# Performance work log

Measured on AMD Instinct MI355X. Metric: run time of the kernel, lower is better.

The kernel has to match this reference:

```python
import jax, jax.numpy as jnp
import numpy as np

DIM = 768
HEADS = 12
HEAD_DIM = DIM // HEADS
EPS = 1e-5

def setup_inputs() -> dict:
    key = jax.random.key(0)
    ks = jax.random.split(key, 12)
    s = 1.0 / np.sqrt(DIM)
    x = jax.random.normal(ks[0], (4, 2048, DIM), dtype=jnp.float32)
    Wq = jax.random.uniform(ks[1], (DIM, DIM), jnp.float32, -s, s)
    bq = jnp.zeros((DIM,), jnp.float32)
    Wk = jax.random.uniform(ks[2], (DIM, DIM), jnp.float32, -s, s)
    bk = jnp.zeros((DIM,), jnp.float32)
    Wv = jax.random.uniform(ks[3], (DIM, DIM), jnp.float32, -s, s)
    bv = jnp.zeros((DIM,), jnp.float32)
    W1 = jax.random.uniform(ks[4], (DIM, 2 * DIM), jnp.float32, -s, s)
    b1 = jnp.zeros((2 * DIM,), jnp.float32)
    s2 = 1.0 / np.sqrt(2 * DIM)
    W2 = jax.random.uniform(ks[5], (2 * DIM, DIM), jnp.float32, -s2, s2)
    b2 = jnp.zeros((DIM,), jnp.float32)
    gamma = jnp.ones((DIM,), jnp.float32)
    beta = jnp.zeros((DIM,), jnp.float32)
    return {"x": x, "Wq": Wq, "bq": bq, "Wk": Wk, "bk": bk, "Wv": Wv, "bv": bv,
            "W1": W1, "b1": b1, "W2": W2, "b2": b2, "gamma": gamma, "beta": beta}

def reference(x, Wq, bq, Wk, bk, Wv, bv, W1, b1, W2, b2, gamma, beta):
    B, S, _ = x.shape
    # QKV projections -> (B, H, S, Dh)
    q = (x @ Wq + bq).reshape(B, S, HEADS, HEAD_DIM).transpose(0, 2, 1, 3)
    k = (x @ Wk + bk).reshape(B, S, HEADS, HEAD_DIM).transpose(0, 2, 1, 3)
    v = (x @ Wv + bv).reshape(B, S, HEADS, HEAD_DIM).transpose(0, 2, 1, 3)
    scores = jnp.einsum('bhqd,bhkd->bhqk', q, k) / jnp.sqrt(jnp.float32(HEAD_DIM))
    attn = jax.nn.softmax(scores, axis=-1)  # dropout is identity in eval
    ctx = jnp.einsum('bhqk,bhkd->bhqd', attn, v)
    ctx = ctx.transpose(0, 2, 1, 3).reshape(B, S, DIM)
    # MLP
    out = jax.nn.relu(ctx @ W1 + b1) @ W2 + b2
    # residual + LayerNorm
    h = x + out
    mu = jnp.mean(h, axis=-1, keepdims=True)
    var = jnp.mean(jnp.square(h - mu), axis=-1, keepdims=True)
    return (h - mu) * jax.lax.rsqrt(var + EPS) * gamma + beta
```

## Files before the change

### kernel.cpp

```cpp
#include <hip/hip_runtime.h>
#include <stdint.h>

#define DIM 768
#define HDIM 64
#define NHEADS 12
#define SEQ 2048
#define BATCH 4
#define NTOK (BATCH*SEQ)
#define FF 1536
#define QSCALE 0.1803368801111204f

typedef __bf16 bf16x8 __attribute__((ext_vector_type(8)));
typedef float f32x4 __attribute__((ext_vector_type(4)));
typedef unsigned short u16;
typedef unsigned int u32;

static __device__ __forceinline__ u16 f2bf(float f) {
  u32 u = __float_as_uint(f);
  u32 r = (u + 0x7fffu + ((u >> 16) & 1u)) >> 16;
  return (u16)r;
}

static __device__ __forceinline__ void async16(const void* g, void* l) {
  __builtin_amdgcn_global_load_lds(
      (const __attribute__((address_space(1))) u32*)g,
      (__attribute__((address_space(3))) u32*)l, 16, 0, 0);
}


__global__ void conv_bf16(const float* __restrict__ in, u16* __restrict__ out, int n) {
  int i = (blockIdx.x * 256 + threadIdx.x) * 4;
  if (i < n) {
    float4 f = *(const float4*)(in + i);
    uint2 o;
    o.x = (u32)f2bf(f.x) | ((u32)f2bf(f.y) << 16);
    o.y = (u32)f2bf(f.z) | ((u32)f2bf(f.w) << 16);
    *(uint2*)(out + i) = o;
  }
}

__global__ void prep_weights(const float* __restrict__ Wq, const float* __restrict__ Wk,
                             const float* __restrict__ Wv, const float* __restrict__ W1,
                             const float* __restrict__ W2, const float* __restrict__ bq,
                             const float* __restrict__ bk, const float* __restrict__ bv,
                             u16* __restrict__ Wqkvt, u16* __restrict__ W1t,
                             u16* __restrict__ W2t, float* __restrict__ bqkv) {
  const int bid = blockIdx.x;
  if (bid >= 4032) {
    int i = (bid - 4032) * 256 + threadIdx.x;
    if (i < DIM) bqkv[i] = bq[i];
    else if (i < 2 * DIM) bqkv[i] = bk[i - DIM];
    else if (i < 3 * DIM) bqkv[i] = bv[i - 2 * DIM];
    return;
  }
  const float* W; u16* dst; int K, N, tile;
  if (bid < 1728) {
    int z = bid / 576, t2 = bid - z * 576;
    W = z == 0 ? Wq : (z == 1 ? Wk : Wv);
    dst = Wqkvt + (size_t)z * DIM * DIM; K = DIM; N = DIM; tile = t2;
  } else if (bid < 2880) {
    W = W1; dst = W1t; K = DIM; N = FF; tile = bid - 1728;
  } else {
    W = W2; dst = W2t; K = FF; N = DIM; tile = bid - 2880;
  }
  const int ntx = N / 32;
  const int k0 = (tile / ntx) * 32, n0 = (tile - (tile / ntx) * ntx) * 32;
  __shared__ float t32[32][33];
  const int tx = threadIdx.x & 31, ty = threadIdx.x >> 5;
#pragma unroll
  for (int i = 0; i < 4; i++)
    t32[ty + 8 * i][tx] = W[(size_t)(k0 + ty + 8 * i) * N + n0 + tx];
  __syncthreads();
#pragma unroll
  for (int i = 0; i < 4; i++)
    dst[(size_t)(n0 + ty + 8 * i) * K + k0 + tx] = f2bf(t32[tx][ty + 8 * i]);
}


template<int MODE, int NT>
__launch_bounds__(256, 3)
__global__ void gemm128(const u16* __restrict__ A, const u16* __restrict__ Bt,
                        const float* __restrict__ bias, void* __restrict__ outp,
                        int K) {
  __shared__ u16 sA[128 * 64];
  __shared__ u16 sB[128 * 64];
  const int t = threadIdx.x;
  const int w = t >> 6;
  const int lane = t & 63;
  const int quad = lane >> 4;
  const int l15 = lane & 15;

  const int fid = blockIdx.x;
  const int xcd = fid & 7;
  const int j = fid >> 3;
  const int m0 = (xcd + 8 * (j / NT)) * 128;
  const int n0 = (j % NT) * 128;

  const int wr = (w & 1) * 64;
  const int wc = (w >> 1) * 64;

  f32x4 acc[4][4];
#pragma unroll
  for (int i = 0; i < 4; i++)
#pragma unroll
    for (int jj = 0; jj < 4; jj++) acc[i][jj] = (f32x4){0.f, 0.f, 0.f, 0.f};

  const int rowA = lane >> 3;
  const int colSw = ((lane & 7) ^ rowA) * 8;

  for (int k0 = 0; k0 < K; k0 += 64) {
    __syncthreads();
#pragma unroll
    for (int jj = 0; jj < 4; jj++) {
      int r0 = (jj * 4 + w) * 8;
      async16(A + (size_t)(m0 + r0 + rowA) * K + k0 + colSw, sA + r0 * 64);
      async16(Bt + (size_t)(n0 + r0 + rowA) * K + k0 + colSw, sB + r0 * 64);
    }
    __builtin_amdgcn_s_waitcnt(0);
    __syncthreads();
#pragma unroll
    for (int ks = 0; ks < 64; ks += 32) {
      bf16x8 a[4], b[4];
#pragma unroll
      for (int i = 0; i < 4; i++)
        a[i] = *(const bf16x8*)(sA + (wr + i * 16 + l15) * 64 +
                                ((((ks >> 3) + quad) ^ (l15 & 7)) * 8));
#pragma unroll
      for (int jj = 0; jj < 4; jj++)
        b[jj] = *(const bf16x8*)(sB + (wc + jj * 16 + l15) * 64 +
                                 ((((ks >> 3) + quad) ^ (l15 & 7)) * 8));
#pragma unroll
      for (int i = 0; i < 4; i++)
#pragma unroll
        for (int jj = 0; jj < 4; jj++)
          acc[i][jj] = __builtin_amdgcn_mfma_f32_16x16x32_bf16(a[i], b[jj], acc[i][jj], 0, 0, 0);
    }
  }

#pragma unroll
  for (int i = 0; i < 4; i++) {
#pragma unroll
    for (int jj = 0; jj < 4; jj++) {
#pragma unroll
      for (int r = 0; r < 4; r++) {
        int m = m0 + wr + i * 16 + quad * 4 + r;
        int n = n0 + wc + jj * 16 + l15;
        float v = acc[i][jj][r] + bias[n];
        if (MODE == 5) {
          int b = m >> 11, s = m & 2047;
          u16* o = (u16*)outp;
          if (n < DIM) {
            int h = n >> 6, d = n & 63;
            o[(((size_t)(b * NHEADS + h) * SEQ + s) << 6) + d] = f2bf(v * QSCALE);
          } else if (n < 2 * DIM) {
            int nn = n - DIM, h = nn >> 6, d = nn & 63;
            o[(size_t)NTOK * DIM + (((size_t)(b * NHEADS + h) * SEQ + s) << 6) + d] = f2bf(v);
          } else {
            int nn = n - 2 * DIM, h = nn >> 6, d = nn & 63;
            o[2 * (size_t)NTOK * DIM + ((size_t)(b * NHEADS + h) * HDIM + d) * SEQ + s] = f2bf(v);
          }
        } else if (MODE == 3) {
          ((u16*)outp)[(size_t)m * FF + n] = f2bf(fmaxf(v, 0.f));
        } else {
          ((float*)outp)[(size_t)m * DIM + n] = v;
        }
      }
    }
  }
}


__launch_bounds__(256, 3)
__global__ void attn(const u16* __restrict__ Q, const u16* __restrict__ Kb,
                     const u16* __restrict__ Vt, u16* __restrict__ Ctx) {
  __shared__ u16 sK[128 * 64];
  __shared__ u16 sV[64 * 128];
  __shared__ u16 sP[4][32 * 64];
  const int t = threadIdx.x, w = t >> 6, lane = t & 63;
  const int quad = lane >> 4, l15 = lane & 15;

  const int fid = blockIdx.x;
  const int xcd = fid & 7;
  const int idx = fid >> 3;
  const int bh = xcd + 8 * (idx >> 4);
  const int qb = idx & 15;
  const size_t qkbase = (size_t)bh * SEQ * HDIM;
  const int q0 = qb * 128 + w * 32;

  bf16x8 qf[2][2];
#pragma unroll
  for (int i = 0; i < 2; i++)
#pragma unroll
    for (int ks = 0; ks < 2; ks++)
      qf[i][ks] = *(const bf16x8*)(Q + qkbase + (size_t)(q0 + i * 16 + l15) * HDIM +
                                   ks * 32 + quad * 8);

  f32x4 o[2][4];
#pragma unroll
  for (int i = 0; i < 2; i++)
#pragma unroll
    for (int di = 0; di < 4; di++) o[i][di] = (f32x4){0.f, 0.f, 0.f, 0.f};
  float rs[2] = {0.f, 0.f};

  const int rowK = lane >> 3;
  const int colKsw = ((lane & 7) ^ rowK) * 8;
  const int rowVl = lane >> 4;
  const int chV = lane & 15;
  const int swz = l15 & 7;

  for (int kt = 0; kt < SEQ / 128; kt++) {
    __syncthreads();
#pragma unroll
    for (int j = 0; j < 4; j++) {
      int rk = (j * 4 + w) * 8;
      async16(Kb + qkbase + (size_t)(kt * 128 + rk + rowK) * HDIM + colKsw, sK + rk * 64);
      int rv = (j * 4 + w) * 4;
      int rV = rv + rowVl;
      int cV = (chV ^ (rV & 15)) * 8;
      async16(Vt + qkbase + (size_t)rV * SEQ + kt * 128 + cV, sV + rv * 128);
    }
    __builtin_amdgcn_s_waitcnt(0);
    __syncthreads();

    u16* pw = sP[w];
#pragma unroll
    for (int hh = 0; hh < 2; hh++) {
      f32x4 sc[2][4];
#pragma unroll
      for (int n4 = 0; n4 < 4; n4++) {
        int kr = (hh * 4 + n4) * 16;
        bf16x8 a0 = *(const bf16x8*)(sK + (kr + l15) * 64 + ((quad ^ swz) * 8));
        bf16x8 a1 = *(const bf16x8*)(sK + (kr + l15) * 64 + (((4 + quad) ^ swz) * 8));
#pragma unroll
        for (int i = 0; i < 2; i++) {
          f32x4 c = (f32x4){0.f, 0.f, 0.f, 0.f};
          c = __builtin_amdgcn_mfma_f32_16x16x32_bf16(a0, qf[i][0], c, 0, 0, 0);
          c = __builtin_amdgcn_mfma_f32_16x16x32_bf16(a1, qf[i][1], c, 0, 0, 0);
          sc[i][n4] = c;
        }
      }
#pragma unroll
      for (int i = 0; i < 2; i++) {
        int row = i * 16 + l15;
#pragma unroll
        for (int n4 = 0; n4 < 4; n4++) {
          float p0 = __builtin_amdgcn_exp2f(sc[i][n4][0]);
          float p1 = __builtin_amdgcn_exp2f(sc[i][n4][1]);
          float p2 = __builtin_amdgcn_exp2f(sc[i][n4][2]);
          float p3 = __builtin_amdgcn_exp2f(sc[i][n4][3]);
          rs[i] += (p0 + p1) + (p2 + p3);
          u32 lo = __builtin_amdgcn_perm(__float_as_uint(p1) + 0x8000u,
                                         __float_as_uint(p0) + 0x8000u, 0x07060302u);
          u32 hi = __builtin_amdgcn_perm(__float_as_uint(p3) + 0x8000u,
                                         __float_as_uint(p2) + 0x8000u, 0x07060302u);
          int cp = (n4 * 2 + (quad >> 1)) ^ swz;
          *(uint2*)(pw + row * 64 + cp * 8 + (quad & 1) * 4) = (uint2){lo, hi};
        }
      }
#pragma unroll
      for (int ks = 0; ks < 2; ks++) {
        bf16x8 ap[2];
#pragma unroll
        for (int i = 0; i < 2; i++) {
          int row = i * 16 + l15;
          int cp = (ks * 4 + quad) ^ swz;
          ap[i] = *(const bf16x8*)(pw + row * 64 + cp * 8);
        }
#pragma unroll
        for (int di = 0; di < 4; di++) {
          bf16x8 b = *(const bf16x8*)(sV + (di * 16 + l15) * 128 +
                                      (((hh * 8 + ks * 4 + quad) ^ l15) * 8));
          o[0][di] = __builtin_amdgcn_mfma_f32_16x16x32_bf16(ap[0], b, o[0][di], 0, 0, 0);
          o[1][di] = __builtin_amdgcn_mfma_f32_16x16x32_bf16(ap[1], b, o[1][di], 0, 0, 0);
        }
      }
    }
  }

  float rsum[2];
#pragma unroll
  for (int i = 0; i < 2; i++) {
    float s = rs[i];
    s += __shfl_xor(s, 16);
    s += __shfl_xor(s, 32);
    rsum[i] = s;
  }
  int b = bh / NHEADS, h = bh - b * NHEADS;
#pragma unroll
  for (int i = 0; i < 2; i++) {
#pragma unroll
    for (int r = 0; r < 4; r++) {
      float inv = 1.f / __shfl(rsum[i], quad * 4 + r);
      int q = q0 + i * 16 + quad * 4 + r;
      size_t base = (size_t)(b * SEQ + q) * DIM + h * HDIM;
#pragma unroll
      for (int di = 0; di < 4; di++)
        Ctx[base + di * 16 + l15] = f2bf(o[i][di][r] * inv);
    }
  }
}


__launch_bounds__(256)
__global__ void ln_kernel(const float* __restrict__ x, const float* __restrict__ y,
                          const float* __restrict__ gamma, const float* __restrict__ beta,
                          float* __restrict__ out) {
  const int tok = blockIdx.x * 4 + (threadIdx.x >> 6);
  const int lane = threadIdx.x & 63;
  const float4* X = (const float4*)(x + (size_t)tok * DIM);
  const float4* Y = (const float4*)(y + (size_t)tok * DIM);
  const float4* G = (const float4*)gamma;
  const float4* Bt = (const float4*)beta;
  float4* O = (float4*)(out + (size_t)tok * DIM);

  float4 h[3];
  float s = 0.f;
#pragma unroll
  for (int i = 0; i < 3; i++) {
    float4 a = X[i * 64 + lane], b = Y[i * 64 + lane];
    h[i].x = a.x + b.x; h[i].y = a.y + b.y; h[i].z = a.z + b.z; h[i].w = a.w + b.w;
    s += h[i].x + h[i].y + h[i].z + h[i].w;
  }
#pragma unroll
  for (int off = 32; off >= 1; off >>= 1) s += __shfl_xor(s, off);
  float mu = s * (1.f / DIM);
  float v = 0.f;
#pragma unroll
  for (int i = 0; i < 3; i++) {
    h[i].x -= mu; h[i].y -= mu; h[i].z -= mu; h[i].w -= mu;
    v += h[i].x * h[i].x + h[i].y * h[i].y + h[i].z * h[i].z + h[i].w * h[i].w;
  }
#pragma unroll
  for (int off = 32; off >= 1; off >>= 1) v += __shfl_xor(v, off);
  float rstd = rsqrtf(v * (1.f / DIM) + 1e-5f);
#pragma unroll
  for (int i = 0; i < 3; i++) {
    float4 g = G[i * 64 + lane], bt = Bt[i * 64 + lane];
    float4 r;
    r.x = h[i].x * rstd * g.x + bt.x;
    r.y = h[i].y * rstd * g.y + bt.y;
    r.z = h[i].z * rstd * g.z + bt.z;
    r.w = h[i].w * rstd * g.w + bt.w;
    O[i * 64 + lane] = r;
  }
}


extern "C" void kernel_launch(void* const* d_in, const int* in_sizes, int n_in,
                              void* d_out, int out_size, void* d_ws, size_t ws_size,
                              hipStream_t stream) {
  const float* x  = (const float*)d_in[0];
  const float* Wq = (const float*)d_in[1];
  const float* bq = (const float*)d_in[2];
  const float* Wk = (const float*)d_in[3];
  const float* bk = (const float*)d_in[4];
  const float* Wv = (const float*)d_in[5];
  const float* bv = (const float*)d_in[6];
  const float* W1 = (const float*)d_in[7];
  const float* b1 = (const float*)d_in[8];
  const float* W2 = (const float*)d_in[9];
  const float* b2 = (const float*)d_in[10];
  const float* gamma = (const float*)d_in[11];
  const float* beta  = (const float*)d_in[12];

  char* ws = (char*)d_ws;
  u16* xb   = (u16*)ws;           ws += (size_t)NTOK * DIM * 2;
  u16* Wqkvt = (u16*)ws;          ws += (size_t)DIM * DIM * 3 * 2;
  u16* W1t  = (u16*)ws;           ws += (size_t)DIM * FF * 2;
  u16* W2t  = (u16*)ws;           ws += (size_t)DIM * FF * 2;
  float* bqkv = (float*)ws;       ws += (size_t)3 * DIM * 4;
  u16* Qb   = (u16*)ws;           ws += (size_t)NTOK * DIM * 2;
  u16* Kbf  = (u16*)ws;           ws += (size_t)NTOK * DIM * 2;
  u16* Vtb  = (u16*)ws;           ws += (size_t)NTOK * DIM * 2;
  u16* Ctx  = (u16*)ws;           ws += (size_t)NTOK * DIM * 2;
  u16* H1   = (u16*)ws;           ws += (size_t)NTOK * FF * 2;
  float* Y2 = (float*)ws;         ws += (size_t)NTOK * DIM * 4;

  conv_bf16<<<(NTOK * DIM) / 1024, 256, 0, stream>>>(x, xb, NTOK * DIM);
  prep_weights<<<4041, 256, 0, stream>>>(Wq, Wk, Wv, W1, W2, bq, bk, bv,
                                         Wqkvt, W1t, W2t, bqkv);

  gemm128<5, 18><<<1152, 256, 0, stream>>>(xb, Wqkvt, bqkv, Qb, DIM);

  attn<<<768, 256, 0, stream>>>(Qb, Kbf, Vtb, Ctx);

  gemm128<3, 12><<<768, 256, 0, stream>>>(Ctx, W1t, b1, H1, DIM);
  gemm128<4, 6><<<384, 256, 0, stream>>>(H1, W2t, b2, Y2, FF);

  ln_kernel<<<NTOK / 4, 256, 0, stream>>>(x, Y2, gamma, beta, (float*)d_out);
}
```

Before: 309.7 us.

## Double-buffer K/V tiles in attention with async prefetch and MFMA priority

Restructures the attention main loop to use 64-key tiles in double-buffered shared memory, prefetching the next K/V tile with async global-to-LDS loads while the current one is computed. This replaces the load-wait-compute pattern that fully exposed memory latency each iteration. It also raises wave priority around the MFMA phases and swaps the manual bf16 rounding for the packed v_cvt_pk_bf16_f32 instruction. The cost is twice as many loop iterations and barriers, and correctness relies on the hand-written vmcnt wait counts.

```diff
diff --git a/kernel.cpp b/kernel.cpp
--- a/kernel.cpp
+++ b/kernel.cpp
@@ -173,8 +173,8 @@
 __launch_bounds__(256, 3)
 __global__ void attn(const u16* __restrict__ Q, const u16* __restrict__ Kb,
                      const u16* __restrict__ Vt, u16* __restrict__ Ctx) {
-  __shared__ u16 sK[128 * 64];
-  __shared__ u16 sV[64 * 128];
+  __shared__ u16 sK[2][64 * 64];
+  __shared__ u16 sV[2][64 * 64];
   __shared__ u16 sP[4][32 * 64];
   const int t = threadIdx.x, w = t >> 6, lane = t & 63;
   const int quad = lane >> 4, l15 = lane & 15;
@@ -204,78 +204,92 @@
 
   const int rowK = lane >> 3;
   const int colKsw = ((lane & 7) ^ rowK) * 8;
-  const int rowVl = lane >> 4;
-  const int chV = lane & 15;
   const int swz = l15 & 7;
 
-  for (int kt = 0; kt < SEQ / 128; kt++) {
-    __syncthreads();
-#pragma unroll
-    for (int j = 0; j < 4; j++) {
-      int rk = (j * 4 + w) * 8;
-      async16(Kb + qkbase + (size_t)(kt * 128 + rk + rowK) * HDIM + colKsw, sK + rk * 64);
-      int rv = (j * 4 + w) * 4;
-      int rV = rv + rowVl;
-      int cV = (chV ^ (rV & 15)) * 8;
-      async16(Vt + qkbase + (size_t)rV * SEQ + kt * 128 + cV, sV + rv * 128);
-    }
-    __builtin_amdgcn_s_waitcnt(0);
-    __syncthreads();
-
+#define STAGE(kt, b) do {                                                          \
+    int rr0 = w * 8, rr1 = (4 + w) * 8;                                            \
+    async16(Kb + qkbase + (size_t)((kt) * 64 + rr0 + rowK) * HDIM + colKsw,        \
+            sK[b] + rr0 * 64);                                                     \
+    async16(Vt + qkbase + (size_t)(rr0 + rowK) * SEQ + (kt) * 64 + colKsw,         \
+            sV[b] + rr0 * 64);                                                     \
+    async16(Kb + qkbase + (size_t)((kt) * 64 + rr1 + rowK) * HDIM + colKsw,        \
+            sK[b] + rr1 * 64);                                                     \
+    async16(Vt + qkbase + (size_t)(rr1 + rowK) * SEQ + (kt) * 64 + colKsw,         \
+            sV[b] + rr1 * 64);                                                     \
+  } while (0)
+
+  auto compute = [&](int cur) {
+    const u16* kb = sK[cur];
+    const u16* vb = sV[cur];
     u16* pw = sP[w];
-#pragma unroll
-    for (int hh = 0; hh < 2; hh++) {
-      f32x4 sc[2][4];
+
+    f32x4 sc[2][4];
+    __builtin_amdgcn_s_setprio(1);
+#pragma unroll
+    for (int n4 = 0; n4 < 4; n4++) {
+      int kr = n4 * 16;
+      bf16x8 a0 = *(const bf16x8*)(kb + (kr + l15) * 64 + ((quad ^ swz) * 8));
+      bf16x8 a1 = *(const bf16x8*)(kb + (kr + l15) * 64 + (((4 + quad) ^ swz) * 8));
+#pragma unroll
+      for (int i = 0; i < 2; i++) {
+        f32x4 c = (f32x4){0.f, 0.f, 0.f, 0.f};
+        c = __builtin_amdgcn_mfma_f32_16x16x32_bf16(a0, qf[i][0], c, 0, 0, 0);
+        c = __builtin_amdgcn_mfma_f32_16x16x32_bf16(a1, qf[i][1], c, 0, 0, 0);
+        sc[i][n4] = c;
+      }
+    }
+    __builtin_amdgcn_s_setprio(0);
+
+#pragma unroll
+    for (int i = 0; i < 2; i++) {
+      int row = i * 16 + l15;
 #pragma unroll
       for (int n4 = 0; n4 < 4; n4++) {
-        int kr = (hh * 4 + n4) * 16;
-        bf16x8 a0 = *(const bf16x8*)(sK + (kr + l15) * 64 + ((quad ^ swz) * 8));
-        bf16x8 a1 = *(const bf16x8*)(sK + (kr + l15) * 64 + (((4 + quad) ^ swz) * 8));
-#pragma unroll
-        for (int i = 0; i < 2; i++) {
-          f32x4 c = (f32x4){0.f, 0.f, 0.f, 0.f};
-          c = __builtin_amdgcn_mfma_f32_16x16x32_bf16(a0, qf[i][0], c, 0, 0, 0);
-          c = __builtin_amdgcn_mfma_f32_16x16x32_bf16(a1, qf[i][1], c, 0, 0, 0);
-          sc[i][n4] = c;
-        }
+        float p0 = __builtin_amdgcn_exp2f(sc[i][n4][0]);
+        float p1 = __builtin_amdgcn_exp2f(sc[i][n4][1]);
+        float p2 = __builtin_amdgcn_exp2f(sc[i][n4][2]);
+        float p3 = __builtin_amdgcn_exp2f(sc[i][n4][3]);
+        rs[i] += (p0 + p1) + (p2 + p3);
+        u32 lo, hi;
+        asm("v_cvt_pk_bf16_f32 %0, %1, %2" : "=v"(lo) : "v"(p0), "v"(p1));
+        asm("v_cvt_pk_bf16_f32 %0, %1, %2" : "=v"(hi) : "v"(p2), "v"(p3));
+        int cp = (n4 * 2 + (quad >> 1)) ^ swz;
+        *(uint2*)(pw + row * 64 + cp * 8 + (quad & 1) * 4) = (uint2){lo, hi};
       }
-#pragma unroll
-      for (int i = 0; i < 2; i++) {
-        int row = i * 16 + l15;
-#pragma unroll
-        for (int n4 = 0; n4 < 4; n4++) {
-          float p0 = __builtin_amdgcn_exp2f(sc[i][n4][0]);
-          float p1 = __builtin_amdgcn_exp2f(sc[i][n4][1]);
-          float p2 = __builtin_amdgcn_exp2f(sc[i][n4][2]);
-          float p3 = __builtin_amdgcn_exp2f(sc[i][n4][3]);
-          rs[i] += (p0 + p1) + (p2 + p3);
-          u32 lo = __builtin_amdgcn_perm(__float_as_uint(p1) + 0x8000u,
-                                         __float_as_uint(p0) + 0x8000u, 0x07060302u);
-          u32 hi = __builtin_amdgcn_perm(__float_as_uint(p3) + 0x8000u,
-                                         __float_as_uint(p2) + 0x8000u, 0x07060302u);
-          int cp = (n4 * 2 + (quad >> 1)) ^ swz;
-          *(uint2*)(pw + row * 64 + cp * 8 + (quad & 1) * 4) = (uint2){lo, hi};
-        }
+    }
+
+    __builtin_amdgcn_s_setprio(1);
+#pragma unroll
+    for (int ks = 0; ks < 2; ks++) {
+      bf16x8 ap[2];
+#pragma unroll
+      for (int i = 0; i < 2; i++)
+        ap[i] = *(const bf16x8*)(pw + (i * 16 + l15) * 64 + (((ks * 4 + quad) ^ swz) * 8));
+#pragma unroll
+      for (int di = 0; di < 4; di++) {
+        bf16x8 b = *(const bf16x8*)(vb + (di * 16 + l15) * 64 +
+                                    (((ks * 4 + quad) ^ swz) * 8));
+        o[0][di] = __builtin_amdgcn_mfma_f32_16x16x32_bf16(ap[0], b, o[0][di], 0, 0, 0);
+        o[1][di] = __builtin_amdgcn_mfma_f32_16x16x32_bf16(ap[1], b, o[1][di], 0, 0, 0);
       }
-#pragma unroll
-      for (int ks = 0; ks < 2; ks++) {
-        bf16x8 ap[2];
-#pragma unroll
-        for (int i = 0; i < 2; i++) {
-          int row = i * 16 + l15;
-          int cp = (ks * 4 + quad) ^ swz;
-          ap[i] = *(const bf16x8*)(pw + row * 64 + cp * 8);
-        }
-#pragma unroll
-        for (int di = 0; di < 4; di++) {
-          bf16x8 b = *(const bf16x8*)(sV + (di * 16 + l15) * 128 +
-                                      (((hh * 8 + ks * 4 + quad) ^ l15) * 8));
-          o[0][di] = __builtin_amdgcn_mfma_f32_16x16x32_bf16(ap[0], b, o[0][di], 0, 0, 0);
-          o[1][di] = __builtin_amdgcn_mfma_f32_16x16x32_bf16(ap[1], b, o[1][di], 0, 0, 0);
-        }
-      }
-    }
-  }
+    }
+    __builtin_amdgcn_s_setprio(0);
+  };
+
+  STAGE(0, 0);
+  int cur = 0;
+  for (int kt = 0; kt < SEQ / 64 - 1; kt++) {
+    STAGE(kt + 1, cur ^ 1);
+    asm volatile("s_waitcnt vmcnt(4)" ::: "memory");
+    __builtin_amdgcn_s_barrier();
+    compute(cur);
+    __builtin_amdgcn_s_barrier();
+    cur ^= 1;
+  }
+  asm volatile("s_waitcnt vmcnt(0)" ::: "memory");
+  __builtin_amdgcn_s_barrier();
+  compute(cur);
+#undef STAGE
 
   float rsum[2];
 #pragma unroll
```

After: 285.5 us. 1.08x faster.
